# Kernel tuning notes

Hardware: AMD Instinct MI355X
Metric: run time of the kernel (lower is better)

## Reference

```python
import jax, jax.numpy as jnp
import numpy as np

NEG_SLOPE = 0.2  # PyG GATConv default negative_slope
BN_EPS = 1e-5


def gat_layer(x, src, dst, W, b, a_src, a_dst, heads, out_ch, concat):
    # x: [N, Fin]; W: [Fin, heads*out_ch]; a_src/a_dst: [heads, out_ch]
    N = x.shape[0]
    h = (x @ W).reshape(N, heads, out_ch)
    s = (h * a_src).sum(-1)            # [N, H]
    d = (h * a_dst).sum(-1)            # [N, H]
    e = jax.nn.leaky_relu(s[src] + d[dst], NEG_SLOPE)   # [E, H]
    # segment softmax over incoming edges of each destination node
    m = jax.ops.segment_max(e, dst, num_segments=N)
    ex = jnp.exp(e - m[dst])
    denom = jax.ops.segment_sum(ex, dst, num_segments=N)
    alpha = ex / (denom[dst] + 1e-16)                   # [E, H]
    out = jax.ops.segment_sum(alpha[:, :, None] * h[src], dst, num_segments=N)  # [N,H,C]
    out = out.reshape(N, heads * out_ch) if concat else out.mean(axis=1)
    return out + b


def batchnorm(x, gamma, beta):
    mu = x.mean(axis=0)
    var = x.var(axis=0)
    return gamma * (x - mu) * jax.lax.rsqrt(var + BN_EPS) + beta


def setup_inputs() -> dict:
    key = jax.random.key(0)
    ks = jax.random.split(key, 24)
    N, E, Fin, Hd, heads, C = 50000, 800000, 128, 64, 4, 2
    wdim = Hd * heads  # 256
    inp = {
        'x': jax.random.normal(ks[0], (N, Fin), jnp.float32),
        'edge_index': jax.random.randint(ks[1], (2, E), 0, N, jnp.int64),
    }
    def glorot(k, shape):
        fan = shape[0] + shape[-1]
        return jax.random.normal(k, shape, jnp.float32) * np.sqrt(2.0 / fan)
    # layer 0: Fin -> heads x Hd (concat)
    inp['W0'] = glorot(ks[2], (Fin, wdim)); inp['b0'] = jnp.zeros((wdim,), jnp.float32)
    inp['asrc0'] = glorot(ks[3], (heads, Hd)); inp['adst0'] = glorot(ks[4], (heads, Hd))
    inp['g0'] = jnp.ones((wdim,), jnp.float32); inp['be0'] = jnp.zeros((wdim,), jnp.float32)
    # layer 1: wdim -> heads x Hd (concat)
    inp['W1'] = glorot(ks[5], (wdim, wdim)); inp['b1'] = jnp.zeros((wdim,), jnp.float32)
    inp['asrc1'] = glorot(ks[6], (heads, Hd)); inp['adst1'] = glorot(ks[7], (heads, Hd))
    inp['g1'] = jnp.ones((wdim,), jnp.float32); inp['be1'] = jnp.zeros((wdim,), jnp.float32)
    # layer 2: wdim -> 1 head x Hd (no concat)
    inp['W2'] = glorot(ks[8], (wdim, Hd)); inp['b2'] = jnp.zeros((Hd,), jnp.float32)
    inp['asrc2'] = glorot(ks[9], (1, Hd)); inp['adst2'] = glorot(ks[10], (1, Hd))
    inp['g2'] = jnp.ones((Hd,), jnp.float32); inp['be2'] = jnp.zeros((Hd,), jnp.float32)
    # classifier: Linear(2*Hd, Hd) -> ReLU -> Linear(Hd, C)
    inp['Wc1'] = glorot(ks[11], (2 * Hd, Hd)); inp['bc1'] = jnp.zeros((Hd,), jnp.float32)
    inp['Wc2'] = glorot(ks[12], (Hd, C)); inp['bc2'] = jnp.zeros((C,), jnp.float32)
    return inp


def reference(x, edge_index, W0, b0, asrc0, adst0, g0, be0,
              W1, b1, asrc1, adst1, g1, be1,
              W2, b2, asrc2, adst2, g2, be2,
              Wc1, bc1, Wc2, bc2):
    N = x.shape[0]
    # add self-loops (PyG GATConv default)
    loops = jnp.arange(N, dtype=edge_index.dtype)
    src = jnp.concatenate([edge_index[0], loops])
    dst = jnp.concatenate([edge_index[1], loops])
    heads, Hd = asrc0.shape[0], asrc0.shape[1]

    h = gat_layer(x, src, dst, W0, b0, asrc0, adst0, heads, Hd, True)
    h = jax.nn.relu(batchnorm(h, g0, be0))
    h = gat_layer(h, src, dst, W1, b1, asrc1, adst1, heads, Hd, True)
    h = jax.nn.relu(batchnorm(h, g1, be1))
    h = gat_layer(h, src, dst, W2, b2, asrc2, adst2, 1, Hd, False)
    h = jax.nn.relu(batchnorm(h, g2, be2))

    pooled = jnp.concatenate([h.mean(axis=0, keepdims=True),
                              h.max(axis=0, keepdims=True)], axis=1)  # [1, 2*Hd]
    z = jax.nn.relu(pooled @ Wc1 + bc1)
    return z @ Wc2 + bc2  # [1, num_classes]
```

## Files before the change

### kernel.cpp

```cpp
#include <hip/hip_runtime.h>


typedef unsigned int uint;
typedef unsigned short ushort;

#define NEG_SLOPE 0.2f
#define BN_EPS 1e-5f
#define NB_RED 256

__device__ __forceinline__ float bf2f(uint u) { return __uint_as_float(u << 16); }
__device__ __forceinline__ ushort f2bf(float f) {
    uint u = __float_as_uint(f);
    u += 0x7fff + ((u >> 16) & 1);
    return (ushort)(u >> 16);
}
__device__ __forceinline__ float lrelu(float x) { return x > 0.f ? x : NEG_SLOPE * x; }


__global__ void prep_kernel(const float* __restrict__ x, ushort* __restrict__ xb,
                            int total_real, int total_pad,
                            const float* __restrict__ W0, ushort* __restrict__ w0t,
                            const float* __restrict__ W1, ushort* __restrict__ w1t,
                            const float* __restrict__ W2, ushort* __restrict__ w2t,
                            const int* __restrict__ ei, int* __restrict__ deg, int E) {
    int i = blockIdx.x * blockDim.x + threadIdx.x;
    if (i < total_pad) {
        xb[i] = (i < total_real) ? f2bf(x[i]) : (ushort)0;
        return;
    }
    int j = i - total_pad;
    if (j < 32768) {
        int n = j / 128, k = j - n * 128;
        w0t[j] = f2bf(W0[(size_t)k * 256 + n]);
        return;
    }
    j -= 32768;
    if (j < 65536) {
        int n = j / 256, k = j - n * 256;
        w1t[j] = f2bf(W1[(size_t)k * 256 + n]);
        return;
    }
    j -= 65536;
    if (j < 16384) {
        int n = j / 256, k = j - n * 256;
        w2t[j] = f2bf(W2[(size_t)k * 64 + n]);
        return;
    }
    j -= 16384;
    if (j < E) atomicAdd(&deg[ei[E + j]], 1);
}


__global__ void scan_part(const int* __restrict__ deg, int* __restrict__ offsets,
                          int* __restrict__ bsum, int N) {
    __shared__ int sh[256];
    int t = threadIdx.x;
    int base = blockIdx.x * 1024 + t * 4;
    int v0 = (base + 0 < N) ? deg[base + 0] : 0;
    int v1 = (base + 1 < N) ? deg[base + 1] : 0;
    int v2 = (base + 2 < N) ? deg[base + 2] : 0;
    int v3 = (base + 3 < N) ? deg[base + 3] : 0;
    int s = v0 + v1 + v2 + v3;
    sh[t] = s;
    __syncthreads();
    for (int off = 1; off < 256; off <<= 1) {
        int y = (t >= off) ? sh[t - off] : 0;
        __syncthreads();
        sh[t] += y;
        __syncthreads();
    }
    int p = sh[t] - s;
    if (base + 0 < N) offsets[base + 0] = p;
    p += v0;
    if (base + 1 < N) offsets[base + 1] = p;
    p += v1;
    if (base + 2 < N) offsets[base + 2] = p;
    p += v2;
    if (base + 3 < N) offsets[base + 3] = p;
    if (t == 255) bsum[blockIdx.x] = sh[255];
}

__global__ void scan_top(const int* __restrict__ bsum, int* __restrict__ bexcl,
                         int nb, int* __restrict__ offsets, int N) {
    if (threadIdx.x == 0) {
        int run = 0;
        for (int b = 0; b < nb; ++b) { bexcl[b] = run; run += bsum[b]; }
        offsets[N] = run;
    }
}

__global__ void scan_add(int* __restrict__ offsets, int* __restrict__ cursor,
                         const int* __restrict__ bexcl, int N) {
    int add = bexcl[blockIdx.x];
    int base = blockIdx.x * 1024 + threadIdx.x * 4;
#pragma unroll
    for (int k = 0; k < 4; ++k) {
        int i = base + k;
        if (i < N) { int v = offsets[i] + add; offsets[i] = v; cursor[i] = v; }
    }
}

__global__ void scatter_kernel(const int* __restrict__ ei, int* __restrict__ cursor,
                               int* __restrict__ srcs, int E) {
    int e = blockIdx.x * blockDim.x + threadIdx.x;
    if (e < E) {
        int s = ei[e];
        int d = ei[E + e];
        int p = atomicAdd(&cursor[d], 1);
        srcs[p] = s;
    }
}


typedef __attribute__((ext_vector_type(8))) short bf16x8;
typedef __attribute__((ext_vector_type(4))) float floatx4;

template <int BN, int H>
__launch_bounds__(256)
__global__ void mfma_gemm_bt(const ushort* __restrict__ A, const ushort* __restrict__ Bt,
                             ushort* __restrict__ C, const float* __restrict__ asrc,
                             const float* __restrict__ adst, float* __restrict__ sv,
                             float* __restrict__ dv, int K, int Nn) {
    constexpr int WCOLS = (BN == 128) ? 2 : 1;
    constexpr int WROWS = 4 / WCOLS;
    constexpr int MT = 128 / (WROWS * 16);
    constexpr int NT = BN / (WCOLS * 16);
    constexpr int BCALLS = (BN * 32 * 2) / 4096;

    __shared__ ushort As[128 * 32];
    __shared__ ushort Bs[BN * 32];

    int t = threadIdx.x;
    int w = t >> 6, l = t & 63;
    int row0 = blockIdx.x * 128;
    int col0 = blockIdx.y * BN;
    int wr = (w / WCOLS) * (MT * 16);
    int wc = (w % WCOLS) * (NT * 16);

    floatx4 acc[MT][NT];
#pragma unroll
    for (int mi = 0; mi < MT; ++mi)
#pragma unroll
        for (int ni = 0; ni < NT; ++ni)
#pragma unroll
            for (int r = 0; r < 4; ++r) acc[mi][ni][r] = 0.f;

    int mrow = l & 15;
    int kc = (l >> 4) * 8;

    for (int kt = 0; kt < K; kt += 32) {
#pragma unroll
        for (int c = 0; c < 2; ++c) {
            int idx = c * 256 + t;
            const ushort* gp = A + (size_t)(row0 + (idx >> 2)) * K + kt + (idx & 3) * 8;
            __builtin_amdgcn_global_load_lds(
                (const __attribute__((address_space(1))) void*)gp,
                (__attribute__((address_space(3))) void*)(As + (idx & ~63) * 8),
                16, 0, 0);
        }
#pragma unroll
        for (int c = 0; c < BCALLS; ++c) {
            int idx = c * 256 + t;
            const ushort* gp = Bt + (size_t)(col0 + (idx >> 2)) * K + kt + (idx & 3) * 8;
            __builtin_amdgcn_global_load_lds(
                (const __attribute__((address_space(1))) void*)gp,
                (__attribute__((address_space(3))) void*)(Bs + (idx & ~63) * 8),
                16, 0, 0);
        }
        __syncthreads();

        bf16x8 af[MT], bfr[NT];
#pragma unroll
        for (int mi = 0; mi < MT; ++mi)
            af[mi] = *(const bf16x8*)&As[(wr + mi * 16 + mrow) * 32 + kc];
#pragma unroll
        for (int ni = 0; ni < NT; ++ni)
            bfr[ni] = *(const bf16x8*)&Bs[(wc + ni * 16 + mrow) * 32 + kc];
#pragma unroll
        for (int mi = 0; mi < MT; ++mi)
#pragma unroll
            for (int ni = 0; ni < NT; ++ni)
                acc[mi][ni] = __builtin_amdgcn_mfma_f32_16x16x32_bf16(
                    af[mi], bfr[ni], acc[mi][ni], 0, 0, 0);
        __syncthreads();
    }

#pragma unroll
    for (int mi = 0; mi < MT; ++mi) {
        int rbase = row0 + wr + mi * 16 + (l >> 4) * 4;
#pragma unroll
        for (int ni = 0; ni < NT; ++ni) {
            int col = col0 + wc + ni * 16 + (l & 15);
#pragma unroll
            for (int r = 0; r < 4; ++r)
                C[(size_t)(rbase + r) * Nn + col] = f2bf(acc[mi][ni][r]);
        }
    }

    float av[NT], bv[NT];
#pragma unroll
    for (int ni = 0; ni < NT; ++ni) {
        int ch = col0 + wc + ni * 16 + (l & 15);
        av[ni] = asrc[ch];
        bv[ni] = adst[ch];
    }
    int gh = (col0 + wc) >> 6;
#pragma unroll
    for (int mi = 0; mi < MT; ++mi) {
#pragma unroll
        for (int r = 0; r < 4; ++r) {
            float s = 0.f, d = 0.f;
#pragma unroll
            for (int ni = 0; ni < NT; ++ni) {
                float hv = acc[mi][ni][r];
                s += hv * av[ni];
                d += hv * bv[ni];
            }
#pragma unroll
            for (int m = 8; m >= 1; m >>= 1) {
                s += __shfl_xor(s, m);
                d += __shfl_xor(d, m);
            }
            if ((l & 15) == 0) {
                int row = row0 + wr + mi * 16 + (l >> 4) * 4 + r;
                sv[row * H + gh] = s;
                dv[row * H + gh] = d;
            }
        }
    }
}


__launch_bounds__(128)
__global__ void agg4_kernel(const ushort* __restrict__ hb, const float* __restrict__ sv,
                            const float* __restrict__ dv, const int* __restrict__ offsets,
                            const int* __restrict__ srcs, const float* __restrict__ bias,
                            ushort* __restrict__ zb, int N) {
    __shared__ float lsum[4][256];
    __shared__ float lden[4][4];

    int i = blockIdx.x;
    int t = threadIdx.x;
    int grp = t >> 5, gl = t & 31;
    int head = gl >> 3;
    int beg = offsets[i], end = offsets[i + 1];

    float d_i = dv[i * 4 + head];
    float ax[8] = {};
    float den = 0.f;

    int j = beg + grp;
    int srcn = (j < end) ? srcs[j] : 0;
    while (j < end) {
        float sval = sv[srcn * 4 + head];
        uint4 q = *(const uint4*)&hb[(size_t)srcn * 256 + gl * 8];
        int jn = j + 4;
        int srcn_n = (jn < end) ? srcs[jn] : 0;
        float wgt = __expf(fminf(lrelu(sval + d_i), 60.f));
        den += wgt;
        uint pr[4] = {q.x, q.y, q.z, q.w};
#pragma unroll
        for (int k = 0; k < 4; ++k) {
            ax[2 * k]     += wgt * bf2f(pr[k] & 0xffffu);
            ax[2 * k + 1] += wgt * bf2f(pr[k] >> 16);
        }
        j = jn; srcn = srcn_n;
    }

#pragma unroll
    for (int k = 0; k < 8; ++k) lsum[grp][gl * 8 + k] = ax[k];
    if ((gl & 7) == 0) lden[grp][head] = den;
    __syncthreads();

    int h = t >> 5;
    float wself = __expf(fminf(lrelu(sv[i * 4 + h] + dv[i * 4 + h]), 60.f));
    float dtot = lden[0][h] + lden[1][h] + lden[2][h] + lden[3][h] + wself + 1e-16f;
    float rden = 1.f / dtot;
    uint p = *(const uint*)&hb[(size_t)i * 256 + 2 * t];
    float a0 = lsum[0][2 * t] + lsum[1][2 * t] + lsum[2][2 * t] + lsum[3][2 * t]
             + wself * bf2f(p & 0xffffu);
    float a1 = lsum[0][2 * t + 1] + lsum[1][2 * t + 1] + lsum[2][2 * t + 1]
             + lsum[3][2 * t + 1] + wself * bf2f(p >> 16);
    a0 = a0 * rden + bias[2 * t];
    a1 = a1 * rden + bias[2 * t + 1];
    *(uint*)&zb[(size_t)i * 256 + 2 * t] = (uint)f2bf(a0) | ((uint)f2bf(a1) << 16);
}


__launch_bounds__(64)
__global__ void agg1_kernel(const ushort* __restrict__ hb, const float* __restrict__ sv,
                            const float* __restrict__ dv, const int* __restrict__ offsets,
                            const int* __restrict__ srcs, const float* __restrict__ bias,
                            ushort* __restrict__ zb, int N) {
    int i = blockIdx.x;
    int l = threadIdx.x;
    int grp = l >> 4, gl = l & 15;
    int beg = offsets[i], end = offsets[i + 1];

    float d_i = dv[i];
    float ax[4] = {};
    float den = 0.f;

    int j = beg + grp;
    int srcn = (j < end) ? srcs[j] : 0;
    while (j < end) {
        float sval = sv[srcn];
        uint2 q = *(const uint2*)&hb[(size_t)srcn * 64 + gl * 4];
        int jn = j + 4;
        int srcn_n = (jn < end) ? srcs[jn] : 0;
        float wgt = __expf(fminf(lrelu(sval + d_i), 60.f));
        den += wgt;
        ax[0] += wgt * bf2f(q.x & 0xffffu);
        ax[1] += wgt * bf2f(q.x >> 16);
        ax[2] += wgt * bf2f(q.y & 0xffffu);
        ax[3] += wgt * bf2f(q.y >> 16);
        j = jn; srcn = srcn_n;
    }

#pragma unroll
    for (int k = 0; k < 4; ++k) {
        ax[k] += __shfl_xor(ax[k], 16);
        ax[k] += __shfl_xor(ax[k], 32);
    }
    den += __shfl_xor(den, 16);
    den += __shfl_xor(den, 32);

    if (l < 16) {
        float wself = __expf(fminf(lrelu(sv[i] + d_i), 60.f));
        float rden = 1.f / (den + wself + 1e-16f);
        uint2 q = *(const uint2*)&hb[(size_t)i * 64 + gl * 4];
        float a0 = (ax[0] + wself * bf2f(q.x & 0xffffu)) * rden + bias[gl * 4 + 0];
        float a1 = (ax[1] + wself * bf2f(q.x >> 16)) * rden + bias[gl * 4 + 1];
        float a2 = (ax[2] + wself * bf2f(q.y & 0xffffu)) * rden + bias[gl * 4 + 2];
        float a3 = (ax[3] + wself * bf2f(q.y >> 16)) * rden + bias[gl * 4 + 3];
        uint2 o;
        o.x = (uint)f2bf(a0) | ((uint)f2bf(a1) << 16);
        o.y = (uint)f2bf(a2) | ((uint)f2bf(a3) << 16);
        *(uint2*)&zb[(size_t)i * 64 + gl * 4] = o;
    }
}


template <int F>
__launch_bounds__(256)
__global__ void bn_stats_kernel(const ushort* __restrict__ x, float* __restrict__ ps,
                                float* __restrict__ pq, int N) {
    constexpr int OCT = F / 8;
    __shared__ float lds_s[F], lds_q[F];
    int t = threadIdx.x;
    if (t < F) { lds_s[t] = 0.f; lds_q[t] = 0.f; }
    __syncthreads();

    float s[8] = {}, q[8] = {};
    int total8 = N * F / 8;
    for (int idx = blockIdx.x * 256 + t; idx < total8; idx += NB_RED * 256) {
        uint4 v = ((const uint4*)x)[idx];
        uint pr[4] = {v.x, v.y, v.z, v.w};
#pragma unroll
        for (int k = 0; k < 4; ++k) {
            float a = bf2f(pr[k] & 0xffffu);
            float b = bf2f(pr[k] >> 16);
            s[2 * k] += a;     q[2 * k] += a * a;
            s[2 * k + 1] += b; q[2 * k + 1] += b * b;
        }
    }
    int co = t % OCT;
#pragma unroll
    for (int j = 0; j < 8; ++j) {
        atomicAdd(&lds_s[co * 8 + j], s[j]);
        atomicAdd(&lds_q[co * 8 + j], q[j]);
    }
    __syncthreads();
    if (t < F) {
        ps[blockIdx.x * F + t] = lds_s[t];
        pq[blockIdx.x * F + t] = lds_q[t];
    }
}

__global__ void bn_final_kernel(const float* __restrict__ ps, const float* __restrict__ pq,
                                const float* __restrict__ g, const float* __restrict__ be,
                                float* __restrict__ scale, float* __restrict__ shift,
                                int N, int F) {
    int t = threadIdx.x;
    if (t < F) {
        float s = 0.f, q = 0.f;
        for (int b = 0; b < NB_RED; ++b) { s += ps[b * F + t]; q += pq[b * F + t]; }
        float mean = s / (float)N;
        float var = q / (float)N - mean * mean;
        float sc = g[t] * rsqrtf(var + BN_EPS);
        scale[t] = sc;
        shift[t] = be[t] - sc * mean;
    }
}

__global__ void bn_apply_kernel(uint* __restrict__ x, const float* __restrict__ scale,
                                const float* __restrict__ shift, int totalPairs, int Fmask) {
    int i = blockIdx.x * blockDim.x + threadIdx.x;
    if (i < totalPairs) {
        uint p = x[i];
        int c0 = (2 * i) & Fmask;
        float v0 = fmaxf(bf2f(p & 0xffffu) * scale[c0] + shift[c0], 0.f);
        float v1 = fmaxf(bf2f(p >> 16) * scale[c0 + 1] + shift[c0 + 1], 0.f);
        x[i] = (uint)f2bf(v0) | ((uint)f2bf(v1) << 16);
    }
}


__launch_bounds__(256)
__global__ void pool_kernel(const ushort* __restrict__ y, const float* __restrict__ scale,
                            const float* __restrict__ shift, float* __restrict__ psum,
                            float* __restrict__ pmax, int N) {
    constexpr int F = 64, OCT = 8;
    __shared__ float lds_s[F];
    __shared__ uint lds_m[F];
    int t = threadIdx.x;
    if (t < F) { lds_s[t] = 0.f; lds_m[t] = 0u; }
    __syncthreads();

    int co = t % OCT;
    float sc[8], sh[8];
#pragma unroll
    for (int j = 0; j < 8; ++j) { sc[j] = scale[co * 8 + j]; sh[j] = shift[co * 8 + j]; }

    float s[8] = {}, m[8] = {};
    int total8 = N * F / 8;
    for (int idx = blockIdx.x * 256 + t; idx < total8; idx += NB_RED * 256) {
        uint4 v = ((const uint4*)y)[idx];
        uint pr[4] = {v.x, v.y, v.z, v.w};
#pragma unroll
        for (int k = 0; k < 4; ++k) {
            float a = fmaxf(bf2f(pr[k] & 0xffffu) * sc[2 * k] + sh[2 * k], 0.f);
            float b = fmaxf(bf2f(pr[k] >> 16) * sc[2 * k + 1] + sh[2 * k + 1], 0.f);
            s[2 * k] += a;     m[2 * k] = fmaxf(m[2 * k], a);
            s[2 * k + 1] += b; m[2 * k + 1] = fmaxf(m[2 * k + 1], b);
        }
    }
#pragma unroll
    for (int j = 0; j < 8; ++j) {
        atomicAdd(&lds_s[co * 8 + j], s[j]);
        atomicMax(&lds_m[co * 8 + j], __float_as_uint(m[j]));
    }
    __syncthreads();
    if (t < F) {
        psum[blockIdx.x * F + t] = lds_s[t];
        pmax[blockIdx.x * F + t] = __uint_as_float(lds_m[t]);
    }
}

__global__ void classify_kernel(const float* __restrict__ psum, const float* __restrict__ pmax,
                                const float* __restrict__ Wc1, const float* __restrict__ bc1,
                                const float* __restrict__ Wc2, const float* __restrict__ bc2,
                                float* __restrict__ out, int N) {
    __shared__ float pooled[128];
    __shared__ float z[64];
    int t = threadIdx.x;
    if (t < 64) {
        float s = 0.f;
        for (int b = 0; b < NB_RED; ++b) s += psum[b * 64 + t];
        pooled[t] = s / (float)N;
    } else {
        int c = t - 64;
        float m = 0.f;
        for (int b = 0; b < NB_RED; ++b) m = fmaxf(m, pmax[b * 64 + c]);
        pooled[t] = m;
    }
    __syncthreads();
    if (t < 64) {
        float a = bc1[t];
        for (int k = 0; k < 128; ++k) a += pooled[k] * Wc1[k * 64 + t];
        z[t] = a > 0.f ? a : 0.f;
    }
    __syncthreads();
    if (t < 2) {
        float a = bc2[t];
        for (int j = 0; j < 64; ++j) a += z[j] * Wc2[j * 2 + t];
        out[t] = a;
    }
}


extern "C" void kernel_launch(void* const* d_in, const int* in_sizes, int n_in,
                              void* d_out, int out_size, void* d_ws, size_t ws_size,
                              hipStream_t stream) {
    const float* x   = (const float*)d_in[0];
    const int*   ei  = (const int*)d_in[1];
    const float* W0  = (const float*)d_in[2];  const float* b0  = (const float*)d_in[3];
    const float* as0 = (const float*)d_in[4];  const float* ad0 = (const float*)d_in[5];
    const float* g0  = (const float*)d_in[6];  const float* be0 = (const float*)d_in[7];
    const float* W1  = (const float*)d_in[8];  const float* b1  = (const float*)d_in[9];
    const float* as1 = (const float*)d_in[10]; const float* ad1 = (const float*)d_in[11];
    const float* g1  = (const float*)d_in[12]; const float* be1 = (const float*)d_in[13];
    const float* W2  = (const float*)d_in[14]; const float* b2  = (const float*)d_in[15];
    const float* as2 = (const float*)d_in[16]; const float* ad2 = (const float*)d_in[17];
    const float* g2  = (const float*)d_in[18]; const float* be2 = (const float*)d_in[19];
    const float* Wc1 = (const float*)d_in[20]; const float* bc1 = (const float*)d_in[21];
    const float* Wc2 = (const float*)d_in[22]; const float* bc2 = (const float*)d_in[23];
    float* out = (float*)d_out;

    const int N = in_sizes[0] / 128;
    const int E = in_sizes[1] / 2;
    const int Mpad = ((N + 127) / 128) * 128;
    const int NB_SCAN = (N + 1023) / 1024;

    char* ws = (char*)d_ws;
    size_t o = 0;
    auto alloc = [&](size_t bytes) -> void* {
        void* p = ws + o;
        o = (o + bytes + 255) & ~(size_t)255;
        return p;
    };
    int*    deg     = (int*)alloc((size_t)N * 4);
    int*    offsets = (int*)alloc((size_t)(N + 1) * 4);
    int*    cursor  = (int*)alloc((size_t)N * 4);
    int*    srcs    = (int*)alloc((size_t)E * 4);
    int*    bsum    = (int*)alloc((size_t)NB_SCAN * 4);
    int*    bexcl   = (int*)alloc((size_t)NB_SCAN * 4);
    ushort* xb      = (ushort*)alloc((size_t)Mpad * 128 * 2);
    ushort* w0t     = (ushort*)alloc((size_t)256 * 128 * 2);
    ushort* w1t     = (ushort*)alloc((size_t)256 * 256 * 2);
    ushort* w2t     = (ushort*)alloc((size_t)64 * 256 * 2);
    ushort* hb      = (ushort*)alloc((size_t)Mpad * 256 * 2);
    ushort* zb      = (ushort*)alloc((size_t)Mpad * 256 * 2);
    float*  sv      = (float*)alloc((size_t)Mpad * 4 * 4);
    float*  dv      = (float*)alloc((size_t)Mpad * 4 * 4);
    float*  ps      = (float*)alloc((size_t)NB_RED * 256 * 4);
    float*  pq      = (float*)alloc((size_t)NB_RED * 256 * 4);
    float*  scale   = (float*)alloc(256 * 4);
    float*  shift   = (float*)alloc(256 * 4);
    float*  psum    = (float*)alloc((size_t)NB_RED * 64 * 4);
    float*  pmax    = (float*)alloc((size_t)NB_RED * 64 * 4);

    hipMemsetAsync(deg, 0, (size_t)N * 4, stream);
    int prep_total = Mpad * 128 + 32768 + 65536 + 16384 + E;
    prep_kernel<<<(prep_total + 255) / 256, 256, 0, stream>>>(
        x, xb, N * 128, Mpad * 128, W0, w0t, W1, w1t, W2, w2t, ei, deg, E);

    scan_part<<<NB_SCAN, 256, 0, stream>>>(deg, offsets, bsum, N);
    scan_top<<<1, 64, 0, stream>>>(bsum, bexcl, NB_SCAN, offsets, N);
    scan_add<<<NB_SCAN, 256, 0, stream>>>(offsets, cursor, bexcl, N);
    scatter_kernel<<<(E + 255) / 256, 256, 0, stream>>>(ei, cursor, srcs, E);

    {
        dim3 gg(Mpad / 128, 2);
        mfma_gemm_bt<128, 4><<<gg, 256, 0, stream>>>(xb, w0t, hb, as0, ad0, sv, dv, 128, 256);
        agg4_kernel<<<N, 128, 0, stream>>>(hb, sv, dv, offsets, srcs, b0, zb, N);
        bn_stats_kernel<256><<<NB_RED, 256, 0, stream>>>(zb, ps, pq, N);
        bn_final_kernel<<<1, 256, 0, stream>>>(ps, pq, g0, be0, scale, shift, N, 256);
        bn_apply_kernel<<<(N * 128 + 255) / 256, 256, 0, stream>>>((uint*)zb, scale, shift,
                                                                   N * 128, 255);
    }
    {
        dim3 gg(Mpad / 128, 2);
        mfma_gemm_bt<128, 4><<<gg, 256, 0, stream>>>(zb, w1t, hb, as1, ad1, sv, dv, 256, 256);
        agg4_kernel<<<N, 128, 0, stream>>>(hb, sv, dv, offsets, srcs, b1, zb, N);
        bn_stats_kernel<256><<<NB_RED, 256, 0, stream>>>(zb, ps, pq, N);
        bn_final_kernel<<<1, 256, 0, stream>>>(ps, pq, g1, be1, scale, shift, N, 256);
        bn_apply_kernel<<<(N * 128 + 255) / 256, 256, 0, stream>>>((uint*)zb, scale, shift,
                                                                   N * 128, 255);
    }
    {
        dim3 gg(Mpad / 128, 1);
        mfma_gemm_bt<64, 1><<<gg, 256, 0, stream>>>(zb, w2t, hb, as2, ad2, sv, dv, 256, 64);
        agg1_kernel<<<N, 64, 0, stream>>>(hb, sv, dv, offsets, srcs, b2, zb, N);
        bn_stats_kernel<64><<<NB_RED, 256, 0, stream>>>(zb, ps, pq, N);
        bn_final_kernel<<<1, 64, 0, stream>>>(ps, pq, g2, be2, scale, shift, N, 64);
    }

    pool_kernel<<<NB_RED, 256, 0, stream>>>(zb, scale, shift, psum, pmax, N);
    classify_kernel<<<1, 128, 0, stream>>>(psum, pmax, Wc1, bc1, Wc2, bc2, out, N);
}
```

Measured before the change: 584.2 us.

## Fuse BN finalize into apply/pool, merge scan kernels, unroll aggregation loops

Folds the BN statistics finalize step into the apply and pool kernels, which now reduce the partial sums themselves and keep scale/shift in shared memory. The scan-top kernel is merged into scan_add, and the reduction block count drops from 256 to 64. The edge aggregation loops in agg4/agg1 now process two edges per iteration to expose more memory-level parallelism, and agg4's shared scratch is padded to avoid bank conflicts. The aim is to cut launch count and latency, at the cost of every block redundantly reducing the BN partials and bsum prefixes.

```diff
diff --git a/kernel.cpp b/kernel.cpp
--- a/kernel.cpp
+++ b/kernel.cpp
@@ -6,7 +6,7 @@
 
 #define NEG_SLOPE 0.2f
 #define BN_EPS 1e-5f
-#define NB_RED 256
+#define NB_RED 64
 
 __device__ __forceinline__ float bf2f(uint u) { return __uint_as_float(u << 16); }
 __device__ __forceinline__ ushort f2bf(float f) {
@@ -80,18 +80,22 @@
     if (t == 255) bsum[blockIdx.x] = sh[255];
 }
 
-__global__ void scan_top(const int* __restrict__ bsum, int* __restrict__ bexcl,
-                         int nb, int* __restrict__ offsets, int N) {
+__global__ void scan_add(int* __restrict__ offsets, int* __restrict__ cursor,
+                         const int* __restrict__ bsum, int N) {
+    __shared__ int sadd;
+    int nb = gridDim.x;
     if (threadIdx.x == 0) {
         int run = 0;
-        for (int b = 0; b < nb; ++b) { bexcl[b] = run; run += bsum[b]; }
-        offsets[N] = run;
-    }
-}
-
-__global__ void scan_add(int* __restrict__ offsets, int* __restrict__ cursor,
-                         const int* __restrict__ bexcl, int N) {
-    int add = bexcl[blockIdx.x];
+        for (int b = 0; b < (int)blockIdx.x; ++b) run += bsum[b];
+        sadd = run;
+        if ((int)blockIdx.x == nb - 1) {
+            int tot = run;
+            for (int b = blockIdx.x; b < nb; ++b) tot += bsum[b];
+            offsets[N] = tot;
+        }
+    }
+    __syncthreads();
+    int add = sadd;
     int base = blockIdx.x * 1024 + threadIdx.x * 4;
 #pragma unroll
     for (int k = 0; k < 4; ++k) {
@@ -236,7 +240,7 @@
                             const float* __restrict__ dv, const int* __restrict__ offsets,
                             const int* __restrict__ srcs, const float* __restrict__ bias,
                             ushort* __restrict__ zb, int N) {
-    __shared__ float lsum[4][256];
+    __shared__ float lsum[4][32 * 9];
     __shared__ float lden[4][4];
 
     int i = blockIdx.x;
@@ -249,41 +253,60 @@
     float ax[8] = {};
     float den = 0.f;
 
-    int j = beg + grp;
-    int srcn = (j < end) ? srcs[j] : 0;
-    while (j < end) {
-        float sval = sv[srcn * 4 + head];
-        uint4 q = *(const uint4*)&hb[(size_t)srcn * 256 + gl * 8];
-        int jn = j + 4;
-        int srcn_n = (jn < end) ? srcs[jn] : 0;
-        float wgt = __expf(fminf(lrelu(sval + d_i), 60.f));
-        den += wgt;
-        uint pr[4] = {q.x, q.y, q.z, q.w};
+    int j0 = beg + grp;
+    int j1 = j0 + 4;
+    while (j1 < end) {
+        int s0 = srcs[j0], s1 = srcs[j1];
+        float sv0 = sv[s0 * 4 + head];
+        float sv1 = sv[s1 * 4 + head];
+        uint4 q0 = *(const uint4*)&hb[(size_t)s0 * 256 + gl * 8];
+        uint4 q1 = *(const uint4*)&hb[(size_t)s1 * 256 + gl * 8];
+        float w0 = __expf(fminf(lrelu(sv0 + d_i), 60.f));
+        float w1 = __expf(fminf(lrelu(sv1 + d_i), 60.f));
+        den += w0 + w1;
+        uint pr0[4] = {q0.x, q0.y, q0.z, q0.w};
+        uint pr1[4] = {q1.x, q1.y, q1.z, q1.w};
 #pragma unroll
         for (int k = 0; k < 4; ++k) {
-            ax[2 * k]     += wgt * bf2f(pr[k] & 0xffffu);
-            ax[2 * k + 1] += wgt * bf2f(pr[k] >> 16);
-        }
-        j = jn; srcn = srcn_n;
-    }
-
-#pragma unroll
-    for (int k = 0; k < 8; ++k) lsum[grp][gl * 8 + k] = ax[k];
+            ax[2 * k]     += w0 * bf2f(pr0[k] & 0xffffu) + w1 * bf2f(pr1[k] & 0xffffu);
+            ax[2 * k + 1] += w0 * bf2f(pr0[k] >> 16)     + w1 * bf2f(pr1[k] >> 16);
+        }
+        j0 += 8; j1 += 8;
+    }
+    if (j0 < end) {
+        int s0 = srcs[j0];
+        float sv0 = sv[s0 * 4 + head];
+        uint4 q0 = *(const uint4*)&hb[(size_t)s0 * 256 + gl * 8];
+        float w0 = __expf(fminf(lrelu(sv0 + d_i), 60.f));
+        den += w0;
+        uint pr0[4] = {q0.x, q0.y, q0.z, q0.w};
+#pragma unroll
+        for (int k = 0; k < 4; ++k) {
+            ax[2 * k]     += w0 * bf2f(pr0[k] & 0xffffu);
+            ax[2 * k + 1] += w0 * bf2f(pr0[k] >> 16);
+        }
+    }
+
+#pragma unroll
+    for (int k = 0; k < 8; ++k) lsum[grp][gl * 9 + k] = ax[k];
     if ((gl & 7) == 0) lden[grp][head] = den;
     __syncthreads();
 
     int h = t >> 5;
+    int c0 = 2 * t, c1 = 2 * t + 1;
+    int i0 = (c0 >> 3) * 9 + (c0 & 7);
+    int i1 = (c1 >> 3) * 9 + (c1 & 7);
     float wself = __expf(fminf(lrelu(sv[i * 4 + h] + dv[i * 4 + h]), 60.f));
     float dtot = lden[0][h] + lden[1][h] + lden[2][h] + lden[3][h] + wself + 1e-16f;
     float rden = 1.f / dtot;
-    uint p = *(const uint*)&hb[(size_t)i * 256 + 2 * t];
-    float a0 = lsum[0][2 * t] + lsum[1][2 * t] + lsum[2][2 * t] + lsum[3][2 * t]
+    uint p = *(const uint*)&hb[(size_t)i * 256 + c0];
+    float a0 = lsum[0][i0] + lsum[1][i0] + lsum[2][i0] + lsum[3][i0]
              + wself * bf2f(p & 0xffffu);
-    float a1 = lsum[0][2 * t + 1] + lsum[1][2 * t + 1] + lsum[2][2 * t + 1]
-             + lsum[3][2 * t + 1] + wself * bf2f(p >> 16);
-    a0 = a0 * rden + bias[2 * t];
-    a1 = a1 * rden + bias[2 * t + 1];
-    *(uint*)&zb[(size_t)i * 256 + 2 * t] = (uint)f2bf(a0) | ((uint)f2bf(a1) << 16);
+    float a1 = lsum[0][i1] + lsum[1][i1] + lsum[2][i1] + lsum[3][i1]
+             + wself * bf2f(p >> 16);
+    a0 = a0 * rden + bias[c0];
+    a1 = a1 * rden + bias[c1];
+    *(uint*)&zb[(size_t)i * 256 + c0] = (uint)f2bf(a0) | ((uint)f2bf(a1) << 16);
 }
 
 
@@ -301,20 +324,32 @@
     float ax[4] = {};
     float den = 0.f;
 
-    int j = beg + grp;
-    int srcn = (j < end) ? srcs[j] : 0;
-    while (j < end) {
-        float sval = sv[srcn];
-        uint2 q = *(const uint2*)&hb[(size_t)srcn * 64 + gl * 4];
-        int jn = j + 4;
-        int srcn_n = (jn < end) ? srcs[jn] : 0;
-        float wgt = __expf(fminf(lrelu(sval + d_i), 60.f));
-        den += wgt;
-        ax[0] += wgt * bf2f(q.x & 0xffffu);
-        ax[1] += wgt * bf2f(q.x >> 16);
-        ax[2] += wgt * bf2f(q.y & 0xffffu);
-        ax[3] += wgt * bf2f(q.y >> 16);
-        j = jn; srcn = srcn_n;
+    int j0 = beg + grp;
+    int j1 = j0 + 4;
+    while (j1 < end) {
+        int s0 = srcs[j0], s1 = srcs[j1];
+        float sv0 = sv[s0], sv1 = sv[s1];
+        uint2 q0 = *(const uint2*)&hb[(size_t)s0 * 64 + gl * 4];
+        uint2 q1 = *(const uint2*)&hb[(size_t)s1 * 64 + gl * 4];
+        float w0 = __expf(fminf(lrelu(sv0 + d_i), 60.f));
+        float w1 = __expf(fminf(lrelu(sv1 + d_i), 60.f));
+        den += w0 + w1;
+        ax[0] += w0 * bf2f(q0.x & 0xffffu) + w1 * bf2f(q1.x & 0xffffu);
+        ax[1] += w0 * bf2f(q0.x >> 16)     + w1 * bf2f(q1.x >> 16);
+        ax[2] += w0 * bf2f(q0.y & 0xffffu) + w1 * bf2f(q1.y & 0xffffu);
+        ax[3] += w0 * bf2f(q0.y >> 16)     + w1 * bf2f(q1.y >> 16);
+        j0 += 8; j1 += 8;
+    }
+    if (j0 < end) {
+        int s0 = srcs[j0];
+        float sv0 = sv[s0];
+        uint2 q0 = *(const uint2*)&hb[(size_t)s0 * 64 + gl * 4];
+        float w0 = __expf(fminf(lrelu(sv0 + d_i), 60.f));
+        den += w0;
+        ax[0] += w0 * bf2f(q0.x & 0xffffu);
+        ax[1] += w0 * bf2f(q0.x >> 16);
+        ax[2] += w0 * bf2f(q0.y & 0xffffu);
+        ax[3] += w0 * bf2f(q0.y >> 16);
     }
 
 #pragma unroll
@@ -377,10 +412,12 @@
     }
 }
 
-__global__ void bn_final_kernel(const float* __restrict__ ps, const float* __restrict__ pq,
-                                const float* __restrict__ g, const float* __restrict__ be,
-                                float* __restrict__ scale, float* __restrict__ shift,
-                                int N, int F) {
+template <int F>
+__launch_bounds__(256)
+__global__ void bn_apply_kernel(uint* __restrict__ x, const float* __restrict__ ps,
+                                const float* __restrict__ pq, const float* __restrict__ g,
+                                const float* __restrict__ be, int N, int totalPairs) {
+    __shared__ float ssc[F], ssh[F];
     int t = threadIdx.x;
     if (t < F) {
         float s = 0.f, q = 0.f;
@@ -388,39 +425,47 @@
         float mean = s / (float)N;
         float var = q / (float)N - mean * mean;
         float sc = g[t] * rsqrtf(var + BN_EPS);
-        scale[t] = sc;
-        shift[t] = be[t] - sc * mean;
-    }
-}
-
-__global__ void bn_apply_kernel(uint* __restrict__ x, const float* __restrict__ scale,
-                                const float* __restrict__ shift, int totalPairs, int Fmask) {
-    int i = blockIdx.x * blockDim.x + threadIdx.x;
-    if (i < totalPairs) {
+        ssc[t] = sc;
+        ssh[t] = be[t] - sc * mean;
+    }
+    __syncthreads();
+    for (int i = blockIdx.x * 256 + t; i < totalPairs; i += gridDim.x * 256) {
         uint p = x[i];
-        int c0 = (2 * i) & Fmask;
-        float v0 = fmaxf(bf2f(p & 0xffffu) * scale[c0] + shift[c0], 0.f);
-        float v1 = fmaxf(bf2f(p >> 16) * scale[c0 + 1] + shift[c0 + 1], 0.f);
+        int c0 = (2 * i) & (F - 1);
+        float v0 = fmaxf(bf2f(p & 0xffffu) * ssc[c0] + ssh[c0], 0.f);
+        float v1 = fmaxf(bf2f(p >> 16) * ssc[c0 + 1] + ssh[c0 + 1], 0.f);
         x[i] = (uint)f2bf(v0) | ((uint)f2bf(v1) << 16);
     }
 }
 
 
 __launch_bounds__(256)
-__global__ void pool_kernel(const ushort* __restrict__ y, const float* __restrict__ scale,
-                            const float* __restrict__ shift, float* __restrict__ psum,
+__global__ void pool_kernel(const ushort* __restrict__ y, const float* __restrict__ ps,
+                            const float* __restrict__ pq, const float* __restrict__ g,
+                            const float* __restrict__ be, float* __restrict__ psum,
                             float* __restrict__ pmax, int N) {
     constexpr int F = 64, OCT = 8;
+    __shared__ float ssc[F], ssh[F];
     __shared__ float lds_s[F];
     __shared__ uint lds_m[F];
     int t = threadIdx.x;
-    if (t < F) { lds_s[t] = 0.f; lds_m[t] = 0u; }
+    if (t < F) {
+        float s = 0.f, q = 0.f;
+        for (int b = 0; b < NB_RED; ++b) { s += ps[b * F + t]; q += pq[b * F + t]; }
+        float mean = s / (float)N;
+        float var = q / (float)N - mean * mean;
+        float sc = g[t] * rsqrtf(var + BN_EPS);
+        ssc[t] = sc;
+        ssh[t] = be[t] - sc * mean;
+        lds_s[t] = 0.f;
+        lds_m[t] = 0u;
+    }
     __syncthreads();
 
     int co = t % OCT;
     float sc[8], sh[8];
 #pragma unroll
-    for (int j = 0; j < 8; ++j) { sc[j] = scale[co * 8 + j]; sh[j] = shift[co * 8 + j]; }
+    for (int j = 0; j < 8; ++j) { sc[j] = ssc[co * 8 + j]; sh[j] = ssh[co * 8 + j]; }
 
     float s[8] = {}, m[8] = {};
     int total8 = N * F / 8;
@@ -514,7 +559,6 @@
     int*    cursor  = (int*)alloc((size_t)N * 4);
     int*    srcs    = (int*)alloc((size_t)E * 4);
     int*    bsum    = (int*)alloc((size_t)NB_SCAN * 4);
-    int*    bexcl   = (int*)alloc((size_t)NB_SCAN * 4);
     ushort* xb      = (ushort*)alloc((size_t)Mpad * 128 * 2);
     ushort* w0t     = (ushort*)alloc((size_t)256 * 128 * 2);
     ushort* w1t     = (ushort*)alloc((size_t)256 * 256 * 2);
@@ -525,8 +569,6 @@
     float*  dv      = (float*)alloc((size_t)Mpad * 4 * 4);
     float*  ps      = (float*)alloc((size_t)NB_RED * 256 * 4);
     float*  pq      = (float*)alloc((size_t)NB_RED * 256 * 4);
-    float*  scale   = (float*)alloc(256 * 4);
-    float*  shift   = (float*)alloc(256 * 4);
     float*  psum    = (float*)alloc((size_t)NB_RED * 64 * 4);
     float*  pmax    = (float*)alloc((size_t)NB_RED * 64 * 4);
 
@@ -536,8 +578,7 @@
         x, xb, N * 128, Mpad * 128, W0, w0t, W1, w1t, W2, w2t, ei, deg, E);
 
     scan_part<<<NB_SCAN, 256, 0, stream>>>(deg, offsets, bsum, N);
-    scan_top<<<1, 64, 0, stream>>>(bsum, bexcl, NB_SCAN, offsets, N);
-    scan_add<<<NB_SCAN, 256, 0, stream>>>(offsets, cursor, bexcl, N);
+    scan_add<<<NB_SCAN, 256, 0, stream>>>(offsets, cursor, bsum, N);
     scatter_kernel<<<(E + 255) / 256, 256, 0, stream>>>(ei, cursor, srcs, E);
 
     {
@@ -545,27 +586,22 @@
         mfma_gemm_bt<128, 4><<<gg, 256, 0, stream>>>(xb, w0t, hb, as0, ad0, sv, dv, 128, 256);
         agg4_kernel<<<N, 128, 0, stream>>>(hb, sv, dv, offsets, srcs, b0, zb, N);
         bn_stats_kernel<256><<<NB_RED, 256, 0, stream>>>(zb, ps, pq, N);
-        bn_final_kernel<<<1, 256, 0, stream>>>(ps, pq, g0, be0, scale, shift, N, 256);
-        bn_apply_kernel<<<(N * 128 + 255) / 256, 256, 0, stream>>>((uint*)zb, scale, shift,
-                                                                   N * 128, 255);
+        bn_apply_kernel<256><<<256, 256, 0, stream>>>((uint*)zb, ps, pq, g0, be0, N, N * 128);
     }
     {
         dim3 gg(Mpad / 128, 2);
         mfma_gemm_bt<128, 4><<<gg, 256, 0, stream>>>(zb, w1t, hb, as1, ad1, sv, dv, 256, 256);
         agg4_kernel<<<N, 128, 0, stream>>>(hb, sv, dv, offsets, srcs, b1, zb, N);
         bn_stats_kernel<256><<<NB_RED, 256, 0, stream>>>(zb, ps, pq, N);
-        bn_final_kernel<<<1, 256, 0, stream>>>(ps, pq, g1, be1, scale, shift, N, 256);
-        bn_apply_kernel<<<(N * 128 + 255) / 256, 256, 0, stream>>>((uint*)zb, scale, shift,
-                                                                   N * 128, 255);
+        bn_apply_kernel<256><<<256, 256, 0, stream>>>((uint*)zb, ps, pq, g1, be1, N, N * 128);
     }
     {
         dim3 gg(Mpad / 128, 1);
         mfma_gemm_bt<64, 1><<<gg, 256, 0, stream>>>(zb, w2t, hb, as2, ad2, sv, dv, 256, 64);
         agg1_kernel<<<N, 64, 0, stream>>>(hb, sv, dv, offsets, srcs, b2, zb, N);
         bn_stats_kernel<64><<<NB_RED, 256, 0, stream>>>(zb, ps, pq, N);
-        bn_final_kernel<<<1, 64, 0, stream>>>(ps, pq, g2, be2, scale, shift, N, 64);
-    }
-
-    pool_kernel<<<NB_RED, 256, 0, stream>>>(zb, scale, shift, psum, pmax, N);
+    }
+
+    pool_kernel<<<NB_RED, 256, 0, stream>>>(zb, ps, pq, g2, be2, psum, pmax, N);
     classify_kernel<<<1, 128, 0, stream>>>(psum, pmax, Wc1, bc1, Wc2, bc2, out, N);
 }
```

After: 610.7 us. +4.5%, slower.
